# Optimization experiments

Hardware: AMD Instinct MI355X
Metric: run time of the kernel (lower is better)

Reference implementation:

```python
import jax, jax.numpy as jnp
import numpy as np

NEG_SLOPE = 0.2
EPS = 1e-16

N_NODES = 100000
N_EDGES = 1600000
IN_CH = 128
HEADS = 4
OUT_CH = 32


def setup_inputs() -> dict:
    key = jax.random.key(0)
    k1, k2, k3, k4, k5 = jax.random.split(key, 5)
    x = jax.random.normal(k1, (N_NODES, IN_CH), dtype=jnp.float32)
    edge_index = jax.random.randint(k2, (2, N_EDGES), 0, N_NODES, dtype=jnp.int64)
    glorot = (6.0 / (IN_CH + HEADS * OUT_CH)) ** 0.5
    W_l = jax.random.uniform(k3, (IN_CH, HEADS * OUT_CH), jnp.float32, -glorot, glorot)
    W_r = jax.random.uniform(k4, (IN_CH, HEADS * OUT_CH), jnp.float32, -glorot, glorot)
    ga = (6.0 / (OUT_CH + 1)) ** 0.5
    att = jax.random.uniform(k5, (HEADS, OUT_CH), jnp.float32, -ga, ga)
    bias = jnp.zeros((HEADS * OUT_CH,), dtype=jnp.float32)
    return {"x": x, "edge_index": edge_index, "W_l": W_l, "W_r": W_r, "att": att, "bias": bias}


def reference(x, edge_index, W_l, W_r, att, bias):
    # GATv2Conv forward (PyG semantics, concat=True, add_self_loops=False)
    N = x.shape[0]
    H, C = att.shape
    src, dst = edge_index[0], edge_index[1]

    x_l = (x @ W_l).reshape(N, H, C)  # source transform
    x_r = (x @ W_r).reshape(N, H, C)  # target transform

    # per-edge attention logits: e_ij = att . leaky_relu(x_l[j] + x_r[i])
    h = x_l[src] + x_r[dst]                      # [E, H, C]
    e = jnp.einsum('ehc,hc->eh', jax.nn.leaky_relu(h, NEG_SLOPE), att)  # [E, H]

    # segment softmax over edges grouped by destination node
    m = jax.ops.segment_max(e, dst, num_segments=N)      # [N, H]
    e_exp = jnp.exp(e - m[dst])                          # [E, H]
    denom = jax.ops.segment_sum(e_exp, dst, num_segments=N)  # [N, H]
    alpha = e_exp / (denom[dst] + EPS)                   # [E, H]

    # attention-weighted message aggregation
    msg = x_l[src] * alpha[:, :, None]                   # [E, H, C]
    out = jax.ops.segment_sum(msg, dst, num_segments=N)  # [N, H, C]
    return out.reshape(N, H * C) + bias
```

## Files before the change

### kernel.cpp

```cpp
#include <hip/hip_runtime.h>
#include <hip/hip_bf16.h>
#include <cstdint>
#include <cstddef>


#define NEG_SLOPE 0.2f
#define EPS_F 1e-16f
#define NRANGE 8
#define NCHUNK 32
#define SORT_B 1024
#define MAX_RSZ 12512

typedef __attribute__((ext_vector_type(8))) short bf16x8;
typedef __attribute__((ext_vector_type(4))) float f32x4;

static __device__ __forceinline__ unsigned f2bf(float f) {
    unsigned u = __float_as_uint(f);
    return (u + 0x7fffu + ((u >> 16) & 1u)) >> 16;
}
static __device__ __forceinline__ float bf2f(unsigned h) {
    return __uint_as_float(h << 16);
}

__global__ __launch_bounds__(SORT_B) void histW_k(const int* __restrict__ dst, int E, int N,
                                                  int rsz, int chunk_e,
                                                  unsigned short* __restrict__ g,
                                                  const float* __restrict__ Wl,
                                                  const float* __restrict__ Wr,
                                                  unsigned short* __restrict__ Wtl,
                                                  unsigned short* __restrict__ Wtr) {
    if (blockIdx.x == NRANGE * NCHUNK) {
        for (int mat = 0; mat < 2; ++mat) {
            const float* W = mat ? Wr : Wl;
            unsigned short* Wt = mat ? Wtr : Wtl;
            for (int i = 0; i < 16; ++i) {
                int idx = (int)threadIdx.x + i * SORT_B;
                int k = idx >> 7, n = idx & 127;
                Wt[n * 128 + k] = (unsigned short)f2bf(W[idx]);
            }
        }
        return;
    }
    __shared__ unsigned lcnt[MAX_RSZ];
    const int r = blockIdx.x & (NRANGE - 1);
    const int c = blockIdx.x >> 3;
    const unsigned r_lo = (unsigned)(r * rsz);
    const int e0 = c * chunk_e;
    const int e1 = min(e0 + chunk_e, E);

    for (int i = threadIdx.x; i < rsz; i += SORT_B) lcnt[i] = 0u;
    __syncthreads();
    for (int e = e0 + (int)threadIdx.x; e < e1; e += SORT_B) {
        unsigned dd = (unsigned)dst[e] - r_lo;
        if (dd < (unsigned)rsz) atomicAdd(&lcnt[dd], 1u);
    }
    __syncthreads();
    unsigned short* gc = g + (size_t)c * N + r_lo;
    int lim = min(rsz, N - (int)r_lo);
    for (int i = threadIdx.x; i < lim; i += SORT_B) gc[i] = (unsigned short)lcnt[i];
}

#define LROW 136
__global__ __launch_bounds__(256) void mfma_gemm_k(const float* __restrict__ A,
                                                   const unsigned short* __restrict__ Wtl,
                                                   const unsigned short* __restrict__ Wtr,
                                                   unsigned short* __restrict__ xl,
                                                   unsigned short* __restrict__ xr,
                                                   int nrows) {
    __shared__ unsigned short As[64 * LROW];
    __shared__ unsigned short Ws[128 * LROW];
    const int tid = threadIdx.x;
    const int wave = tid >> 6, lane = tid & 63;
    const int quad = lane >> 4, m16 = lane & 15;
    const int row0 = blockIdx.x * 64;

#pragma unroll
    for (int i = 0; i < 8; ++i) {
        int idx = tid + i * 256;
        int r = idx >> 5, c4 = idx & 31;
        int gr = row0 + r;
        gr = gr < nrows ? gr : nrows - 1;
        float4 v = *(const float4*)(A + (size_t)gr * 128 + c4 * 4);
        ushort4 b;
        b.x = (unsigned short)f2bf(v.x);
        b.y = (unsigned short)f2bf(v.y);
        b.z = (unsigned short)f2bf(v.z);
        b.w = (unsigned short)f2bf(v.w);
        *(ushort4*)(&As[r * LROW + c4 * 4]) = b;
    }
#pragma unroll
    for (int i = 0; i < 8; ++i) {
        int idx = tid + i * 256;
        int n = idx >> 4, kq = idx & 15;
        *(uint4*)(&Ws[n * LROW + kq * 8]) = *(const uint4*)(Wtl + n * 128 + kq * 8);
    }
    __syncthreads();

    bf16x8 af[4];
#pragma unroll
    for (int ks = 0; ks < 4; ++ks)
        af[ks] = *(const bf16x8*)(&As[(wave * 16 + m16) * LROW + ks * 32 + quad * 8]);

    f32x4 acc[8];
#pragma unroll
    for (int ct = 0; ct < 8; ++ct) acc[ct] = (f32x4){0.f, 0.f, 0.f, 0.f};
#pragma unroll
    for (int ct = 0; ct < 8; ++ct)
#pragma unroll
        for (int ks = 0; ks < 4; ++ks) {
            bf16x8 bf = *(const bf16x8*)(&Ws[(ct * 16 + m16) * LROW + ks * 32 + quad * 8]);
            acc[ct] = __builtin_amdgcn_mfma_f32_16x16x32_bf16(af[ks], bf, acc[ct], 0, 0, 0);
        }
#pragma unroll
    for (int ct = 0; ct < 8; ++ct)
#pragma unroll
        for (int r = 0; r < 4; ++r) {
            int grow = row0 + wave * 16 + quad * 4 + r;
            if (grow < nrows) xl[(size_t)grow * 128 + ct * 16 + m16] = (unsigned short)f2bf(acc[ct][r]);
        }

    __syncthreads();
#pragma unroll
    for (int i = 0; i < 8; ++i) {
        int idx = tid + i * 256;
        int n = idx >> 4, kq = idx & 15;
        *(uint4*)(&Ws[n * LROW + kq * 8]) = *(const uint4*)(Wtr + n * 128 + kq * 8);
    }
    __syncthreads();

#pragma unroll
    for (int ct = 0; ct < 8; ++ct) acc[ct] = (f32x4){0.f, 0.f, 0.f, 0.f};
#pragma unroll
    for (int ct = 0; ct < 8; ++ct)
#pragma unroll
        for (int ks = 0; ks < 4; ++ks) {
            bf16x8 bf = *(const bf16x8*)(&Ws[(ct * 16 + m16) * LROW + ks * 32 + quad * 8]);
            acc[ct] = __builtin_amdgcn_mfma_f32_16x16x32_bf16(af[ks], bf, acc[ct], 0, 0, 0);
        }
#pragma unroll
    for (int ct = 0; ct < 8; ++ct)
#pragma unroll
        for (int r = 0; r < 4; ++r) {
            int grow = row0 + wave * 16 + quad * 4 + r;
            if (grow < nrows) xr[(size_t)grow * 128 + ct * 16 + m16] = (unsigned short)f2bf(acc[ct][r]);
        }
}

__global__ __launch_bounds__(256) void colsum_k(const unsigned short* __restrict__ g, int N,
                                                int* __restrict__ cnt) {
    int d = blockIdx.x * 256 + threadIdx.x;
    if (d >= N) return;
    unsigned s = 0;
#pragma unroll
    for (int c = 0; c < NCHUNK; ++c) s += g[(size_t)c * N + d];
    cnt[d] = (int)s;
}

#define SCAN_B 256
__global__ __launch_bounds__(SCAN_B) void scanA_k(const int* __restrict__ cnt, int n,
                                                  int* __restrict__ row_start,
                                                  int* __restrict__ bsum) {
    const int tid = threadIdx.x, lane = tid & 63, wid = tid >> 6;
    const int g = blockIdx.x * SCAN_B + tid;
    int v = (g < n) ? cnt[g] : 0;
    int inc = v;
#pragma unroll
    for (int d = 1; d < 64; d <<= 1) {
        int t = __shfl_up(inc, d);
        if (lane >= d) inc += t;
    }
    __shared__ int wsum[SCAN_B / 64];
    if (lane == 63) wsum[wid] = inc;
    __syncthreads();
    int add = 0;
    for (int w = 0; w < wid; ++w) add += wsum[w];
    inc += add;
    if (g < n) row_start[g] = inc - v;
    if (tid == SCAN_B - 1) bsum[blockIdx.x] = inc;
}

__global__ __launch_bounds__(512) void scanB_k(int* __restrict__ bsum, int nb) {
    const int tid = threadIdx.x, lane = tid & 63, wid = tid >> 6;
    int v = (tid < nb) ? bsum[tid] : 0;
    int inc = v;
#pragma unroll
    for (int d = 1; d < 64; d <<= 1) {
        int t = __shfl_up(inc, d);
        if (lane >= d) inc += t;
    }
    __shared__ int wsum[8];
    if (lane == 63) wsum[wid] = inc;
    __syncthreads();
    int add = 0;
    for (int w = 0; w < wid; ++w) add += wsum[w];
    inc += add;
    if (tid < nb) bsum[tid] = inc - v;
}

__global__ __launch_bounds__(SCAN_B) void scanC_k(int* __restrict__ row_start,
                                                  const int* __restrict__ bsum,
                                                  int n, int E,
                                                  int* __restrict__ src_sorted) {
    const int g = blockIdx.x * SCAN_B + threadIdx.x;
    if (g < n) row_start[g] += bsum[blockIdx.x];
    if (g == 0) row_start[n] = E;
    if (blockIdx.x == 0 && threadIdx.x < 8) src_sorted[E + threadIdx.x] = 0;
}

__global__ __launch_bounds__(256) void cbase_k(const unsigned short* __restrict__ g,
                                               const int* __restrict__ row_start, int N,
                                               unsigned* __restrict__ base) {
    int d = blockIdx.x * 256 + threadIdx.x;
    if (d >= N) return;
    unsigned run = (unsigned)row_start[d];
#pragma unroll
    for (int c = 0; c < NCHUNK; ++c) {
        base[(size_t)c * N + d] = run;
        run += g[(size_t)c * N + d];
    }
}

__global__ __launch_bounds__(SORT_B) void scat_k(const int* __restrict__ src,
                                                 const int* __restrict__ dst, int E, int N,
                                                 int rsz, int chunk_e,
                                                 const unsigned* __restrict__ base,
                                                 int* __restrict__ src_sorted) {
    __shared__ unsigned lcur[MAX_RSZ];
    const int r = blockIdx.x & (NRANGE - 1);
    const int c = blockIdx.x >> 3;
    const unsigned r_lo = (unsigned)(r * rsz);
    const int e0 = c * chunk_e;
    const int e1 = min(e0 + chunk_e, E);

    const unsigned* bc = base + (size_t)c * N + r_lo;
    int lim = min(rsz, N - (int)r_lo);
    for (int i = threadIdx.x; i < lim; i += SORT_B) lcur[i] = bc[i];
    __syncthreads();

    for (int e = e0 + (int)threadIdx.x; e < e1; e += SORT_B) {
        unsigned dd = (unsigned)dst[e] - r_lo;
        if (dd < (unsigned)rsz) {
            unsigned pos = atomicAdd(&lcur[dd], 1u);
            src_sorted[pos] = src[e] << 8;
        }
    }
}

__global__ __launch_bounds__(256) void agg_k(const unsigned* __restrict__ xlb,
                                             const unsigned* __restrict__ xrb,
                                             const float* __restrict__ att,
                                             const float* __restrict__ bias,
                                             const int* __restrict__ row_start,
                                             const int* __restrict__ src_sorted,
                                             int n, float* __restrict__ out) {
    const int wave = threadIdx.x >> 6;
    const int lane = threadIdx.x & 63;
    const int i = blockIdx.x * 4 + wave;
    if (i >= n) return;

    const int idx  = lane & 31;
    const int half = lane >> 5;
    const int ib   = idx * 8;
    const char* xb = (const char*)xlb;

    uint2 xr2 = *(const uint2*)(xrb + (size_t)i * 64 + idx * 2);
    float xr0 = bf2f(xr2.x & 0xffffu), xr1 = bf2f(xr2.x >> 16);
    float xr2f = bf2f(xr2.y & 0xffffu), xr3 = bf2f(xr2.y >> 16);
    float4 at4 = *(const float4*)(att + idx * 4);

    const int k0 = row_start[i];
    const int k1 = row_start[i + 1];

    float l = 0.f, A0 = 0.f, A1 = 0.f, A2 = 0.f, A3 = 0.f;

    for (int k = k0; k < k1; k += 8) {
        const int kb = k + 4 * half;
        int s[4];
#pragma unroll
        for (int u = 0; u < 4; ++u) s[u] = src_sorted[kb + u];
        uint2 v[4];
#pragma unroll
        for (int u = 0; u < 4; ++u) v[u] = *(const uint2*)(xb + (unsigned)s[u] + ib);
#pragma unroll
        for (int u = 0; u < 4; ++u) {
            float x0 = bf2f(v[u].x & 0xffffu), x1 = bf2f(v[u].x >> 16);
            float x2 = bf2f(v[u].y & 0xffffu), x3 = bf2f(v[u].y >> 16);
            float h0 = x0 + xr0, h1 = x1 + xr1, h2 = x2 + xr2f, h3 = x3 + xr3;
            h0 = fmaxf(h0, NEG_SLOPE * h0);
            h1 = fmaxf(h1, NEG_SLOPE * h1);
            h2 = fmaxf(h2, NEG_SLOPE * h2);
            h3 = fmaxf(h3, NEG_SLOPE * h3);
            float p = fmaf(at4.x, h0, at4.y * h1) + fmaf(at4.z, h2, at4.w * h3);
            p += __shfl_xor(p, 1);
            p += __shfl_xor(p, 2);
            p += __shfl_xor(p, 4);
            float w = (kb + u < k1) ? __expf(p) : 0.f;
            l += w;
            A0 = fmaf(w, x0, A0);
            A1 = fmaf(w, x1, A1);
            A2 = fmaf(w, x2, A2);
            A3 = fmaf(w, x3, A3);
        }
    }

    l  += __shfl_xor(l, 32);
    A0 += __shfl_xor(A0, 32);
    A1 += __shfl_xor(A1, 32);
    A2 += __shfl_xor(A2, 32);
    A3 += __shfl_xor(A3, 32);

    if (half == 0) {
        float inv = 1.f / (l + EPS_F);
        float4 b4 = *(const float4*)(bias + idx * 4);
        float4 o = {fmaf(A0, inv, b4.x), fmaf(A1, inv, b4.y),
                    fmaf(A2, inv, b4.z), fmaf(A3, inv, b4.w)};
        *(float4*)(out + (size_t)i * 128 + idx * 4) = o;
    }
}

extern "C" void kernel_launch(void* const* d_in, const int* in_sizes, int n_in,
                              void* d_out, int out_size, void* d_ws, size_t ws_size,
                              hipStream_t stream) {
    const float* x    = (const float*)d_in[0];
    const int*   ei   = (const int*)d_in[1];
    const float* W_l  = (const float*)d_in[2];
    const float* W_r  = (const float*)d_in[3];
    const float* att  = (const float*)d_in[4];
    const float* bias = (const float*)d_in[5];
    float* out = (float*)d_out;

    const int N = in_sizes[0] / 128;
    const int E = in_sizes[1] / 2;
    const int* src = ei;
    const int* dst = ei + E;

    char* ws = (char*)d_ws;
    size_t off = 0;
    auto alloc = [&](size_t bytes) {
        void* p = ws + off;
        off += (bytes + 15) & ~(size_t)15;
        return p;
    };
    unsigned* xlb       = (unsigned*)alloc((size_t)N * 64 * 4);
    unsigned* xrb       = (unsigned*)alloc((size_t)N * 64 * 4);
    unsigned short* g   = (unsigned short*)alloc((size_t)NCHUNK * N * 2);
    unsigned* base      = (unsigned*)alloc((size_t)NCHUNK * N * 4);
    int* cnt            = (int*)alloc((size_t)N * 4);
    int* row_start      = (int*)alloc((size_t)(N + 1) * 4);
    const int nsb = (N + SCAN_B - 1) / SCAN_B;
    int* bsum           = (int*)alloc((size_t)nsb * 4);
    int* src_sorted     = (int*)alloc((size_t)(E + 8) * 4);
    unsigned short* Wtl = (unsigned short*)alloc((size_t)128 * 128 * 2);
    unsigned short* Wtr = (unsigned short*)alloc((size_t)128 * 128 * 2);
    (void)ws_size;

    const int rsz = (N + NRANGE - 1) / NRANGE;
    const int chunk_e = (E + NCHUNK - 1) / NCHUNK;

    histW_k<<<NRANGE * NCHUNK + 1, SORT_B, 0, stream>>>(dst, E, N, rsz, chunk_e, g,
                                                        W_l, W_r, Wtl, Wtr);

    const int gB = (N + 63) / 64;
    mfma_gemm_k<<<gB, 256, 0, stream>>>(x, Wtl, Wtr,
                                        (unsigned short*)xlb, (unsigned short*)xrb, N);

    colsum_k<<<(N + 255) / 256, 256, 0, stream>>>(g, N, cnt);
    scanA_k<<<nsb, SCAN_B, 0, stream>>>(cnt, N, row_start, bsum);
    scanB_k<<<1, 512, 0, stream>>>(bsum, nsb);
    scanC_k<<<nsb, SCAN_B, 0, stream>>>(row_start, bsum, N, E, src_sorted);
    cbase_k<<<(N + 255) / 256, 256, 0, stream>>>(g, row_start, N, base);

    scat_k<<<NRANGE * NCHUNK, SORT_B, 0, stream>>>(src, dst, E, N, rsz, chunk_e,
                                                   base, src_sorted);

    agg_k<<<(N + 3) / 4, 256, 0, stream>>>(xlb, xrb, att, bias, row_start, src_sorted, N, out);
}
```

Baseline: 289.3 us.

## Fuse column-sum into scan and widen aggregation gathers to 16-byte loads

```diff
diff --git a/kernel.cpp b/kernel.cpp
--- a/kernel.cpp
+++ b/kernel.cpp
@@ -20,6 +20,12 @@
 }
 static __device__ __forceinline__ float bf2f(unsigned h) {
     return __uint_as_float(h << 16);
+}
+static __device__ __forceinline__ float bflo(unsigned u) {
+    return __uint_as_float(u << 16);
+}
+static __device__ __forceinline__ float bfhi(unsigned u) {
+    return __uint_as_float(u & 0xffff0000u);
 }
 
 __global__ __launch_bounds__(SORT_B) void histW_k(const int* __restrict__ dst, int E, int N,
@@ -146,28 +152,24 @@
         }
 }
 
-__global__ __launch_bounds__(256) void colsum_k(const unsigned short* __restrict__ g, int N,
-                                                int* __restrict__ cnt) {
-    int d = blockIdx.x * 256 + threadIdx.x;
-    if (d >= N) return;
-    unsigned s = 0;
-#pragma unroll
-    for (int c = 0; c < NCHUNK; ++c) s += g[(size_t)c * N + d];
-    cnt[d] = (int)s;
-}
-
 #define SCAN_B 256
-__global__ __launch_bounds__(SCAN_B) void scanA_k(const int* __restrict__ cnt, int n,
+__global__ __launch_bounds__(SCAN_B) void scanA_k(const unsigned short* __restrict__ g, int n,
                                                   int* __restrict__ row_start,
                                                   int* __restrict__ bsum) {
     const int tid = threadIdx.x, lane = tid & 63, wid = tid >> 6;
-    const int g = blockIdx.x * SCAN_B + tid;
-    int v = (g < n) ? cnt[g] : 0;
+    const int d = blockIdx.x * SCAN_B + tid;
+    int v = 0;
+    if (d < n) {
+        unsigned s = 0;
+#pragma unroll
+        for (int c = 0; c < NCHUNK; ++c) s += g[(size_t)c * n + d];
+        v = (int)s;
+    }
     int inc = v;
 #pragma unroll
-    for (int d = 1; d < 64; d <<= 1) {
-        int t = __shfl_up(inc, d);
-        if (lane >= d) inc += t;
+    for (int dd = 1; dd < 64; dd <<= 1) {
+        int t = __shfl_up(inc, dd);
+        if (lane >= dd) inc += t;
     }
     __shared__ int wsum[SCAN_B / 64];
     if (lane == 63) wsum[wid] = inc;
@@ -175,7 +177,7 @@
     int add = 0;
     for (int w = 0; w < wid; ++w) add += wsum[w];
     inc += add;
-    if (g < n) row_start[g] = inc - v;
+    if (d < n) row_start[d] = inc - v;
     if (tid == SCAN_B - 1) bsum[blockIdx.x] = inc;
 }
 
@@ -258,63 +260,80 @@
     const int i = blockIdx.x * 4 + wave;
     if (i >= n) return;
 
-    const int idx  = lane & 31;
-    const int half = lane >> 5;
-    const int ib   = idx * 8;
+    const int sub = lane & 15;
+    const int eg  = lane >> 4;
+    const int cb  = sub * 16;
     const char* xb = (const char*)xlb;
 
-    uint2 xr2 = *(const uint2*)(xrb + (size_t)i * 64 + idx * 2);
-    float xr0 = bf2f(xr2.x & 0xffffu), xr1 = bf2f(xr2.x >> 16);
-    float xr2f = bf2f(xr2.y & 0xffffu), xr3 = bf2f(xr2.y >> 16);
-    float4 at4 = *(const float4*)(att + idx * 4);
+    uint4 xrv = *(const uint4*)(xrb + (size_t)i * 64 + sub * 4);
+    const float xr0 = bflo(xrv.x), xr1 = bfhi(xrv.x);
+    const float xr2 = bflo(xrv.y), xr3 = bfhi(xrv.y);
+    const float xr4 = bflo(xrv.z), xr5 = bfhi(xrv.z);
+    const float xr6 = bflo(xrv.w), xr7 = bfhi(xrv.w);
+
+    const float L2E = 1.44269504088896f;
+    float4 atA = *(const float4*)(att + sub * 8);
+    float4 atB = *(const float4*)(att + sub * 8 + 4);
+    atA.x *= L2E; atA.y *= L2E; atA.z *= L2E; atA.w *= L2E;
+    atB.x *= L2E; atB.y *= L2E; atB.z *= L2E; atB.w *= L2E;
 
     const int k0 = row_start[i];
     const int k1 = row_start[i + 1];
 
-    float l = 0.f, A0 = 0.f, A1 = 0.f, A2 = 0.f, A3 = 0.f;
-
-    for (int k = k0; k < k1; k += 8) {
-        const int kb = k + 4 * half;
-        int s[4];
-#pragma unroll
-        for (int u = 0; u < 4; ++u) s[u] = src_sorted[kb + u];
-        uint2 v[4];
-#pragma unroll
-        for (int u = 0; u < 4; ++u) v[u] = *(const uint2*)(xb + (unsigned)s[u] + ib);
-#pragma unroll
-        for (int u = 0; u < 4; ++u) {
-            float x0 = bf2f(v[u].x & 0xffffu), x1 = bf2f(v[u].x >> 16);
-            float x2 = bf2f(v[u].y & 0xffffu), x3 = bf2f(v[u].y >> 16);
-            float h0 = x0 + xr0, h1 = x1 + xr1, h2 = x2 + xr2f, h3 = x3 + xr3;
-            h0 = fmaxf(h0, NEG_SLOPE * h0);
-            h1 = fmaxf(h1, NEG_SLOPE * h1);
-            h2 = fmaxf(h2, NEG_SLOPE * h2);
-            h3 = fmaxf(h3, NEG_SLOPE * h3);
-            float p = fmaf(at4.x, h0, at4.y * h1) + fmaf(at4.z, h2, at4.w * h3);
-            p += __shfl_xor(p, 1);
-            p += __shfl_xor(p, 2);
-            p += __shfl_xor(p, 4);
-            float w = (kb + u < k1) ? __expf(p) : 0.f;
-            l += w;
-            A0 = fmaf(w, x0, A0);
-            A1 = fmaf(w, x1, A1);
-            A2 = fmaf(w, x2, A2);
-            A3 = fmaf(w, x3, A3);
-        }
-    }
-
-    l  += __shfl_xor(l, 32);
-    A0 += __shfl_xor(A0, 32);
-    A1 += __shfl_xor(A1, 32);
-    A2 += __shfl_xor(A2, 32);
-    A3 += __shfl_xor(A3, 32);
-
-    if (half == 0) {
+    float l = 0.f;
+    float A0 = 0.f, A1 = 0.f, A2 = 0.f, A3 = 0.f;
+    float A4 = 0.f, A5 = 0.f, A6 = 0.f, A7 = 0.f;
+
+    for (int k = k0; k < k1; k += 4) {
+        int s = src_sorted[k + eg];
+        uint4 v = *(const uint4*)(xb + (unsigned)s + cb);
+        float x0 = bflo(v.x), x1 = bfhi(v.x);
+        float x2 = bflo(v.y), x3 = bfhi(v.y);
+        float x4 = bflo(v.z), x5 = bfhi(v.z);
+        float x6 = bflo(v.w), x7 = bfhi(v.w);
+        float h0 = x0 + xr0, h1 = x1 + xr1, h2 = x2 + xr2, h3 = x3 + xr3;
+        float h4 = x4 + xr4, h5 = x5 + xr5, h6 = x6 + xr6, h7 = x7 + xr7;
+        float t, p;
+        t = fmaxf(h0, NEG_SLOPE * h0); p = atA.x * t;
+        t = fmaxf(h1, NEG_SLOPE * h1); p = fmaf(atA.y, t, p);
+        t = fmaxf(h2, NEG_SLOPE * h2); p = fmaf(atA.z, t, p);
+        t = fmaxf(h3, NEG_SLOPE * h3); p = fmaf(atA.w, t, p);
+        t = fmaxf(h4, NEG_SLOPE * h4); p = fmaf(atB.x, t, p);
+        t = fmaxf(h5, NEG_SLOPE * h5); p = fmaf(atB.y, t, p);
+        t = fmaxf(h6, NEG_SLOPE * h6); p = fmaf(atB.z, t, p);
+        t = fmaxf(h7, NEG_SLOPE * h7); p = fmaf(atB.w, t, p);
+        p += __shfl_xor(p, 1);
+        p += __shfl_xor(p, 2);
+        float w;
+        asm("v_exp_f32 %0, %1" : "=v"(w) : "v"(p));
+        w = (k + eg < k1) ? w : 0.f;
+        l += w;
+        A0 = fmaf(w, x0, A0); A1 = fmaf(w, x1, A1);
+        A2 = fmaf(w, x2, A2); A3 = fmaf(w, x3, A3);
+        A4 = fmaf(w, x4, A4); A5 = fmaf(w, x5, A5);
+        A6 = fmaf(w, x6, A6); A7 = fmaf(w, x7, A7);
+    }
+
+    l  += __shfl_xor(l, 16);  l  += __shfl_xor(l, 32);
+    A0 += __shfl_xor(A0, 16); A0 += __shfl_xor(A0, 32);
+    A1 += __shfl_xor(A1, 16); A1 += __shfl_xor(A1, 32);
+    A2 += __shfl_xor(A2, 16); A2 += __shfl_xor(A2, 32);
+    A3 += __shfl_xor(A3, 16); A3 += __shfl_xor(A3, 32);
+    A4 += __shfl_xor(A4, 16); A4 += __shfl_xor(A4, 32);
+    A5 += __shfl_xor(A5, 16); A5 += __shfl_xor(A5, 32);
+    A6 += __shfl_xor(A6, 16); A6 += __shfl_xor(A6, 32);
+    A7 += __shfl_xor(A7, 16); A7 += __shfl_xor(A7, 32);
+
+    if (eg == 0) {
         float inv = 1.f / (l + EPS_F);
-        float4 b4 = *(const float4*)(bias + idx * 4);
-        float4 o = {fmaf(A0, inv, b4.x), fmaf(A1, inv, b4.y),
-                    fmaf(A2, inv, b4.z), fmaf(A3, inv, b4.w)};
-        *(float4*)(out + (size_t)i * 128 + idx * 4) = o;
+        float4 b0 = *(const float4*)(bias + sub * 8);
+        float4 b1 = *(const float4*)(bias + sub * 8 + 4);
+        float4 o0 = {fmaf(A0, inv, b0.x), fmaf(A1, inv, b0.y),
+                     fmaf(A2, inv, b0.z), fmaf(A3, inv, b0.w)};
+        float4 o1 = {fmaf(A4, inv, b1.x), fmaf(A5, inv, b1.y),
+                     fmaf(A6, inv, b1.z), fmaf(A7, inv, b1.w)};
+        *(float4*)(out + (size_t)i * 128 + sub * 8)     = o0;
+        *(float4*)(out + (size_t)i * 128 + sub * 8 + 4) = o1;
     }
 }
 
@@ -345,7 +364,6 @@
     unsigned* xrb       = (unsigned*)alloc((size_t)N * 64 * 4);
     unsigned short* g   = (unsigned short*)alloc((size_t)NCHUNK * N * 2);
     unsigned* base      = (unsigned*)alloc((size_t)NCHUNK * N * 4);
-    int* cnt            = (int*)alloc((size_t)N * 4);
     int* row_start      = (int*)alloc((size_t)(N + 1) * 4);
     const int nsb = (N + SCAN_B - 1) / SCAN_B;
     int* bsum           = (int*)alloc((size_t)nsb * 4);
@@ -364,8 +382,7 @@
     mfma_gemm_k<<<gB, 256, 0, stream>>>(x, Wtl, Wtr,
                                         (unsigned short*)xlb, (unsigned short*)xrb, N);
 
-    colsum_k<<<(N + 255) / 256, 256, 0, stream>>>(g, N, cnt);
-    scanA_k<<<nsb, SCAN_B, 0, stream>>>(cnt, N, row_start, bsum);
+    scanA_k<<<nsb, SCAN_B, 0, stream>>>(g, N, row_start, bsum);
     scanB_k<<<1, 512, 0, stream>>>(bsum, nsb);
     scanC_k<<<nsb, SCAN_B, 0, stream>>>(row_start, bsum, N, E, src_sorted);
     cbase_k<<<(N + 255) / 256, 256, 0, stream>>>(g, row_start, N, base);
```

After: 294.1 us. Within noise of the previous version (+1.7%).
